# Optimization experiments

Measured on AMD Instinct MI355X. Metric: run time of the kernel, lower is better.

Reference implementation:

```python
import jax, jax.numpy as jnp
import numpy as np

BN_EPS = 1e-5


def setup_inputs() -> dict:
    key = jax.random.key(0)
    ks = jax.random.split(key, 10)
    B, C, H, W = 8, 512, 64, 64      # batch, in_channels, spatial
    K, V, O = 256, 256, 512          # key_channels, value_channels, out_channels
    s = 0.02
    return {
        "x": jax.random.normal(ks[0], (B, C, H, W), jnp.float32),
        # 1x1 convs are channel matmuls: weight [out_c, in_c]
        "wv": jax.random.normal(ks[1], (V, C), jnp.float32) * s,
        "bv": jax.random.normal(ks[2], (V,), jnp.float32) * s,
        "wk": jax.random.normal(ks[3], (K, C), jnp.float32) * s,
        "bk": jax.random.normal(ks[4], (K,), jnp.float32) * s,
        # BatchNorm2d (inference mode: running stats)
        "gamma": jnp.ones((K,), jnp.float32),
        "beta": jnp.zeros((K,), jnp.float32),
        "rmean": jax.random.normal(ks[5], (K,), jnp.float32) * 0.1,
        "rvar": jax.random.uniform(ks[6], (K,), jnp.float32, 0.5, 1.5),
        # output 1x1 conv W (zero-init in torch; use small random for a useful baseline)
        "wW": jax.random.normal(ks[7], (O, V), jnp.float32) * s,
        "bW": jax.random.normal(ks[8], (O,), jnp.float32) * s,
    }


def reference(x, wv, bv, wk, bk, gamma, beta, rmean, rvar, wW, bW):
    B, C, H, W = x.shape
    N = H * W
    xf = x.reshape(B, C, N)                                   # [B, C, N]

    # f_value: 1x1 conv -> [B, V, N]
    value = jnp.einsum('vc,bcn->bvn', wv, xf) + bv[:, None]

    # f_key (= f_query, shared module): conv1x1 + BN(inference) + ReLU -> [B, K, N]
    k = jnp.einsum('kc,bcn->bkn', wk, xf) + bk[:, None]
    scale = gamma / jnp.sqrt(rvar + BN_EPS)
    k = (k - rmean[:, None]) * scale[:, None] + beta[:, None]
    k = jax.nn.relu(k)

    # sim_map = query^T @ key * K^-0.5; query == key since f_query is f_key
    Kc = k.shape[1]
    sim = jnp.einsum('bkn,bkm->bnm', k, k) * (Kc ** -0.5)     # [B, N, N]
    sim = jax.nn.softmax(sim, axis=-1)

    # context = sim @ value^T -> [B, V, N]
    ctx = jnp.einsum('bnm,bvm->bvn', sim, value)

    # output 1x1 conv W
    out = jnp.einsum('ov,bvn->bon', wW, ctx) + bW[:, None]    # [B, O, N]
    return out.reshape(B, -1, H, W)
```

## Files before the change

kernel.cpp:

```cpp
#include <hip/hip_runtime.h>
#include <hip/hip_bf16.h>
#include <stdint.h>


typedef __bf16 bf16;
typedef bf16 bf16x4 __attribute__((ext_vector_type(4)));
typedef bf16 bf16x8 __attribute__((ext_vector_type(8)));
typedef float f32x4 __attribute__((ext_vector_type(4)));
typedef float f32x16 __attribute__((ext_vector_type(16)));

#define Bb 8
#define Cc 512
#define Nn 4096
#define Kc 256
#define Vv 256
#define Oo 512
#define BN_EPS 1e-5f
#define QSCALE 0.300280601f

static __device__ __forceinline__ f32x16 mfma32(bf16x8 a, bf16x8 b, f32x16 c) {
    return __builtin_amdgcn_mfma_f32_32x32x16_bf16(a, b, c, 0, 0, 0);
}
static __device__ __forceinline__ unsigned cvtpk(float lo, float hi) {
    unsigned r;
    asm("v_cvt_pk_bf16_f32 %0, %1, %2" : "=v"(r) : "v"(lo), "v"(hi));
    return r;
}
#define GLD16(gp, lp) __builtin_amdgcn_global_load_lds( \
    (const __attribute__((address_space(1))) unsigned int*)(gp), \
    (__attribute__((address_space(3))) unsigned int*)(lp), 16, 0, 0)

__global__ __launch_bounds__(256) void prep_kernel(
        const float* __restrict__ wk, const float* __restrict__ wv,
        const float* __restrict__ wW, const float* __restrict__ bk,
        const float* __restrict__ gamma, const float* __restrict__ beta,
        const float* __restrict__ rmean, const float* __restrict__ rvar,
        bf16* __restrict__ wkv, bf16* __restrict__ wWb, float* __restrict__ shift2) {
    int idx = blockIdx.x * 256 + threadIdx.x;
    if (idx < 131072) {
        int kc = idx >> 9;
        float sc = gamma[kc] * rsqrtf(rvar[kc] + BN_EPS);
        wkv[idx] = (bf16)(wk[idx] * sc);
    } else if (idx < 262144) {
        wkv[idx] = (bf16)(wv[idx - 131072]);
    } else if (idx < 393216) {
        int j = idx - 262144;
        wWb[j] = (bf16)(wW[j]);
    } else if (idx < 393472) {
        int kc = idx - 393216;
        float sc = gamma[kc] * rsqrtf(rvar[kc] + BN_EPS);
        shift2[kc] = (bk[kc] - rmean[kc]) * sc + beta[kc];
    }
}

__global__ __launch_bounds__(256, 2) void proj_kernel(
        const float* __restrict__ x, const bf16* __restrict__ wkv,
        const float* __restrict__ shift2, const float* __restrict__ bv,
        bf16* __restrict__ kT, bf16* __restrict__ val) {
    int tile = blockIdx.x;
    int b = tile >> 6, n0 = (tile & 63) * 64;
    int t = threadIdx.x, w = t >> 6, l = t & 63, li = l & 31, hi = l >> 5;
    int nsub = w & 1, ochalf = w >> 1;
    int n = n0 + nsub * 32 + li;
    int ncol = nsub * 32 + li;

    __shared__ float xs[32][65];
    bf16x8 bfr[32];
    int r = t >> 3, sseg = t & 7;
#pragma unroll
    for (int p = 0; p < 16; ++p) {
        const float* src = x + ((size_t)(b * Cc + p * 32 + r)) * Nn + n0 + sseg * 8;
        float4 v0 = *(const float4*)src;
        float4 v1 = *(const float4*)(src + 4);
        if (p) __syncthreads();
        xs[r][sseg * 8 + 0] = v0.x; xs[r][sseg * 8 + 1] = v0.y;
        xs[r][sseg * 8 + 2] = v0.z; xs[r][sseg * 8 + 3] = v0.w;
        xs[r][sseg * 8 + 4] = v1.x; xs[r][sseg * 8 + 5] = v1.y;
        xs[r][sseg * 8 + 6] = v1.z; xs[r][sseg * 8 + 7] = v1.w;
        __syncthreads();
        bf16x8 e0, e1;
#pragma unroll
        for (int j = 0; j < 8; ++j) {
            e0[j] = (bf16)xs[hi * 8 + j][ncol];
            e1[j] = (bf16)xs[16 + hi * 8 + j][ncol];
        }
        bfr[2 * p] = e0;
        bfr[2 * p + 1] = e1;
    }

    f32x16 Z;
#pragma unroll
    for (int rr = 0; rr < 16; ++rr) Z[rr] = 0.f;

    auto writeout = [&](const f32x16& acc, int ocbase) {
        if (ocbase < 256) {
#pragma unroll
            for (int rq = 0; rq < 4; ++rq) {
                int kc0 = ocbase + rq * 8 + hi * 4;
                bf16x4 o;
#pragma unroll
                for (int rr = 0; rr < 4; ++rr) {
                    float v = acc[rq * 4 + rr] + shift2[kc0 + rr];
                    o[rr] = (bf16)(fmaxf(v, 0.f) * QSCALE);
                }
                *(bf16x4*)(kT + ((size_t)(b * Nn + n)) * Kc + kc0) = o;
            }
        } else {
#pragma unroll
            for (int rq = 0; rq < 4; ++rq)
#pragma unroll
                for (int rr = 0; rr < 4; ++rr) {
                    int vc = ocbase - 256 + rq * 8 + hi * 4 + rr;
                    val[((size_t)(b * Vv + vc)) * Nn + n] = (bf16)(acc[rq * 4 + rr] + bv[vc]);
                }
        }
    };

    for (int ocp = 0; ocp < 4; ++ocp) {
        int base0 = ochalf * 256 + ocp * 64;
        const bf16* a0 = wkv + (size_t)(base0 + li) * Cc + hi * 8;
        const bf16* a1 = a0 + (size_t)32 * Cc;
        f32x16 acc0 = mfma32(*(const bf16x8*)(a0), bfr[0], Z);
        f32x16 acc1 = mfma32(*(const bf16x8*)(a1), bfr[0], Z);
#pragma unroll
        for (int cs = 1; cs < 32; ++cs) {
            acc0 = mfma32(*(const bf16x8*)(a0 + cs * 16), bfr[cs], acc0);
            acc1 = mfma32(*(const bf16x8*)(a1 + cs * 16), bfr[cs], acc1);
        }
        writeout(acc0, base0);
        writeout(acc1, base0 + 32);
    }
}

__global__ __launch_bounds__(256, 2) void flash_kernel(
        const bf16* __restrict__ kT, const bf16* __restrict__ val,
        bf16* __restrict__ ctxP, float* __restrict__ ml) {
    __shared__ __align__(16) char lds[65536];
    const int t = threadIdx.x;
    const int b = blockIdx.x;
    const int s = blockIdx.z;
    const int w = t >> 6, l = t & 63, li = l & 31, hi = l >> 5;
    const int n = blockIdx.y * 128 + w * 32 + li;
    const int m0 = s * (Nn / 2);
    const int NT = (Nn / 2) / 32;

    const bf16* kTb  = kT  + (size_t)b * Nn * Kc;
    const bf16* valb = val + (size_t)b * Vv * Nn;

    const bf16* qrow = kTb + (size_t)n * Kc;
    bf16x8 qf[16];
#pragma unroll
    for (int cs = 0; cs < 16; ++cs) qf[cs] = *(const bf16x8*)(qrow + cs * 16 + hi * 8);

    int koff[4];
#pragma unroll
    for (int j = 0; j < 4; ++j) {
        int r = j * 8 + (t >> 5);
        koff[j] = r * Kc + ((t & 31) ^ r) * 8;
    }
    char* kdst = lds + w * 1024;
    char* vdst = lds + 16384 + w * 1024;

    const int kq = li * 512 + ((li ^ hi) << 4);
    const int pv = hi * 4096 + li * 16;

    f32x16 Z;
#pragma unroll
    for (int r = 0; r < 16; ++r) Z[r] = 0.f;
    f32x16 ctx[8];
#pragma unroll
    for (int vc = 0; vc < 8; ++vc) ctx[vc] = Z;
    float M = -1.0e30f, L = 0.f;

    auto STAGE = [&](int tile, int bb) {
        const bf16* kg = kTb + (size_t)(m0 + tile * 32) * Kc;
        const bf16* vg = valb + (size_t)t * Nn + (m0 + tile * 32);
#pragma unroll
        for (int j = 0; j < 4; ++j) GLD16(kg + koff[j], kdst + bb * 32768 + j * 4096);
#pragma unroll
        for (int j = 0; j < 4; ++j) GLD16(vg + j * 8, vdst + bb * 32768 + j * 4096);
    };

    STAGE(0, 0);
    for (int it = 0; it < NT; ++it) {
        const int bb = it & 1;
        if (it + 1 < NT) {
            STAGE(it + 1, bb ^ 1);
            asm volatile("s_waitcnt vmcnt(8)" ::: "memory");
        } else {
            asm volatile("s_waitcnt vmcnt(0)" ::: "memory");
        }
        __builtin_amdgcn_s_barrier();
        __builtin_amdgcn_sched_barrier(0);
        const char* kb = lds + bb * 32768;
        const char* vb = kb + 16384;

        __builtin_amdgcn_s_setprio(1);
        f32x16 S = mfma32(*(const bf16x8*)(kb + kq), qf[0], Z);
#pragma unroll
        for (int cs = 1; cs < 16; ++cs) {
            bf16x8 a0 = *(const bf16x8*)(kb + (kq ^ (cs << 5)));
            S = mfma32(a0, qf[cs], S);
        }
        __builtin_amdgcn_s_setprio(0);

        float m0a = fmaxf(fmaxf(S[0], S[1]), fmaxf(S[2], S[3]));
        float m0b = fmaxf(fmaxf(S[4], S[5]), fmaxf(S[6], S[7]));
        float m0c = fmaxf(fmaxf(S[8], S[9]), fmaxf(S[10], S[11]));
        float m0d = fmaxf(fmaxf(S[12], S[13]), fmaxf(S[14], S[15]));
        float tmax = fmaxf(fmaxf(m0a, m0b), fmaxf(m0c, m0d));
        tmax = fmaxf(tmax, __shfl_xor(tmax, 32, 64));
        if (__any(tmax > M + 8.f)) {
            float newM = fmaxf(M, tmax);
            float alpha = exp2f(M - newM);
            M = newM;
            L *= alpha;
#pragma unroll
            for (int vc = 0; vc < 8; ++vc) ctx[vc] = ctx[vc] * alpha;
        }
#pragma unroll
        for (int r = 0; r < 16; ++r) S[r] = exp2f(S[r] - M);
        float t0 = (S[0] + S[1]) + (S[2] + S[3]);
        float t1 = (S[4] + S[5]) + (S[6] + S[7]);
        float t2 = (S[8] + S[9]) + (S[10] + S[11]);
        float t3 = (S[12] + S[13]) + (S[14] + S[15]);
        float tsum = (t0 + t1) + (t2 + t3);
        tsum += __shfl_xor(tsum, 32, 64);
        L += tsum;

        unsigned c0 = cvtpk(S[0], S[1]),  c1 = cvtpk(S[2], S[3]);
        unsigned c2 = cvtpk(S[4], S[5]),  c3 = cvtpk(S[6], S[7]);
        unsigned c4 = cvtpk(S[8], S[9]),  c5 = cvtpk(S[10], S[11]);
        unsigned c6 = cvtpk(S[12], S[13]), c7 = cvtpk(S[14], S[15]);
        auto r0 = __builtin_amdgcn_permlane32_swap(c0, c2, false, false);
        auto r1 = __builtin_amdgcn_permlane32_swap(c1, c3, false, false);
        auto r2 = __builtin_amdgcn_permlane32_swap(c4, c6, false, false);
        auto r3 = __builtin_amdgcn_permlane32_swap(c5, c7, false, false);
        union U8 { unsigned u[4]; bf16x8 v; } B1, B2;
        B1.u[0] = r0[0]; B1.u[1] = r1[0]; B1.u[2] = r0[1]; B1.u[3] = r1[1];
        B2.u[0] = r2[0]; B2.u[1] = r3[0]; B2.u[2] = r2[1]; B2.u[3] = r3[1];

        __builtin_amdgcn_s_setprio(1);
#pragma unroll
        for (int vc = 0; vc < 8; ++vc) {
            bf16x8 va = *(const bf16x8*)(vb + pv + vc * 512);
            ctx[vc] = mfma32(va, B1.v, ctx[vc]);
        }
#pragma unroll
        for (int vc = 0; vc < 8; ++vc) {
            bf16x8 va = *(const bf16x8*)(vb + pv + 8192 + vc * 512);
            ctx[vc] = mfma32(va, B2.v, ctx[vc]);
        }
        __builtin_amdgcn_s_setprio(0);
        if (it + 1 < NT) {
            __builtin_amdgcn_sched_barrier(0);
            __builtin_amdgcn_s_barrier();
        }
    }

    size_t idx = (size_t)(s * Bb + b) * Nn + n;
    bf16* crow = ctxP + idx * Vv;
#pragma unroll
    for (int vc = 0; vc < 8; ++vc) {
#pragma unroll
        for (int rq = 0; rq < 4; ++rq) {
            bf16x4 o;
#pragma unroll
            for (int r = 0; r < 4; ++r) o[r] = (bf16)ctx[vc][rq * 4 + r];
            *(bf16x4*)(crow + vc * 32 + rq * 8 + hi * 4) = o;
        }
    }
    if (hi == 0) {
        float2 v; v.x = M; v.y = L;
        *(float2*)(ml + idx * 2) = v;
    }
}

__global__ __launch_bounds__(256, 2) void out_kernel(
        const bf16* __restrict__ ctxP, const float* __restrict__ ml,
        const bf16* __restrict__ wWb, const float* __restrict__ bW,
        float* __restrict__ out) {
    int tile = blockIdx.x;
    int b = tile >> 6, n0 = (tile & 63) * 64;
    int t = threadIdx.x, w = t >> 6, l = t & 63, li = l & 31, hi = l >> 5;
    int nsub = w & 1, ochalf = w >> 1;
    int n = n0 + nsub * 32 + li;

    size_t iA = (size_t)b * Nn + n;
    size_t iB = (size_t)(Bb + b) * Nn + n;
    const bf16* ca = ctxP + iA * Vv + hi * 8;
    const bf16* cb = ctxP + iB * Vv + hi * 8;
    float MA = ml[iA * 2], LA = ml[iA * 2 + 1];
    float MB = ml[iB * 2], LB = ml[iB * 2 + 1];
    float Mx = fmaxf(MA, MB);
    float wA = exp2f(MA - Mx), wB = exp2f(MB - Mx);
    float inv = 1.f / (LA * wA + LB * wB);
    float sA = wA * inv, sB = wB * inv;

    bf16x8 bfr[16];
#pragma unroll
    for (int cs = 0; cs < 16; ++cs) {
        bf16x8 fa = *(const bf16x8*)(ca + cs * 16);
        bf16x8 fb = *(const bf16x8*)(cb + cs * 16);
        bf16x8 o;
#pragma unroll
        for (int j = 0; j < 8; ++j)
            o[j] = (bf16)(sA * (float)fa[j] + sB * (float)fb[j]);
        bfr[cs] = o;
    }

    f32x16 Z;
#pragma unroll
    for (int r = 0; r < 16; ++r) Z[r] = 0.f;

    for (int ocp = 0; ocp < 4; ++ocp) {
        int base0 = ochalf * 256 + ocp * 64;
        const bf16* a0 = wWb + (size_t)(base0 + li) * Vv + hi * 8;
        const bf16* a1 = a0 + (size_t)32 * Vv;
        f32x16 acc0 = mfma32(*(const bf16x8*)(a0), bfr[0], Z);
        f32x16 acc1 = mfma32(*(const bf16x8*)(a1), bfr[0], Z);
#pragma unroll
        for (int cs = 1; cs < 16; ++cs) {
            acc0 = mfma32(*(const bf16x8*)(a0 + cs * 16), bfr[cs], acc0);
            acc1 = mfma32(*(const bf16x8*)(a1 + cs * 16), bfr[cs], acc1);
        }
#pragma unroll
        for (int rq = 0; rq < 4; ++rq)
#pragma unroll
            for (int r = 0; r < 4; ++r) {
                int oc0 = base0 + rq * 8 + hi * 4 + r;
                out[((size_t)(b * Oo + oc0)) * Nn + n] = acc0[rq * 4 + r] + bW[oc0];
                int oc1 = oc0 + 32;
                out[((size_t)(b * Oo + oc1)) * Nn + n] = acc1[rq * 4 + r] + bW[oc1];
            }
    }
}

extern "C" void kernel_launch(void* const* d_in, const int* in_sizes, int n_in,
                              void* d_out, int out_size, void* d_ws, size_t ws_size,
                              hipStream_t stream) {
    const float* x     = (const float*)d_in[0];
    const float* wv    = (const float*)d_in[1];
    const float* bv    = (const float*)d_in[2];
    const float* wk    = (const float*)d_in[3];
    const float* bk    = (const float*)d_in[4];
    const float* gamma = (const float*)d_in[5];
    const float* beta  = (const float*)d_in[6];
    const float* rmean = (const float*)d_in[7];
    const float* rvar  = (const float*)d_in[8];
    const float* wW    = (const float*)d_in[9];
    const float* bW    = (const float*)d_in[10];
    float* out = (float*)d_out;

    char* ws = (char*)d_ws;
    bf16*  ctxP   = (bf16*)(ws + 0);
    bf16*  kTp    = (bf16*)(ws + 33554432);
    bf16*  valp   = (bf16*)(ws + 50331648);
    bf16*  wkv    = (bf16*)(ws + 67108864);
    bf16*  wWb    = (bf16*)(ws + 67633152);
    float* shift2 = (float*)(ws + 67895296);
    float* ml     = (float*)(ws + 68157440);

    prep_kernel<<<dim3(1537), dim3(256), 0, stream>>>(wk, wv, wW, bk, gamma, beta,
                                                      rmean, rvar, wkv, wWb, shift2);
    proj_kernel<<<dim3(512), dim3(256), 0, stream>>>(x, wkv, shift2, bv, kTp, valp);
    flash_kernel<<<dim3(8, 32, 2), dim3(256), 0, stream>>>(kTp, valp, ctxP, ml);
    out_kernel<<<dim3(512), dim3(256), 0, stream>>>(ctxP, ml, wWb, bW, out);
}
```

Before: 279.3 us.

## Software-pipeline P·V of previous tile with QK^T of current tile

```diff
diff --git a/kernel.cpp b/kernel.cpp
--- a/kernel.cpp
+++ b/kernel.cpp
@@ -135,7 +135,7 @@
 __global__ __launch_bounds__(256, 2) void flash_kernel(
         const bf16* __restrict__ kT, const bf16* __restrict__ val,
         bf16* __restrict__ ctxP, float* __restrict__ ml) {
-    __shared__ __align__(16) char lds[65536];
+    __shared__ __align__(16) char lds[81920];
     const int t = threadIdx.x;
     const int b = blockIdx.x;
     const int s = blockIdx.z;
@@ -159,7 +159,7 @@
         koff[j] = r * Kc + ((t & 31) ^ r) * 8;
     }
     char* kdst = lds + w * 1024;
-    char* vdst = lds + 16384 + w * 1024;
+    char* vdst = lds + 32768 + w * 1024;
 
     const int kq = li * 512 + ((li ^ hi) << 4);
     const int pv = hi * 4096 + li * 16;
@@ -172,37 +172,58 @@
     for (int vc = 0; vc < 8; ++vc) ctx[vc] = Z;
     float M = -1.0e30f, L = 0.f;
 
-    auto STAGE = [&](int tile, int bb) {
+    union U8 { unsigned u[4]; bf16x8 v; };
+    U8 B1p, B2p;
+#pragma unroll
+    for (int j = 0; j < 4; ++j) { B1p.u[j] = 0u; B2p.u[j] = 0u; }
+
+    auto STAGE = [&](int tile, int kbb, int vbb) {
         const bf16* kg = kTb + (size_t)(m0 + tile * 32) * Kc;
         const bf16* vg = valb + (size_t)t * Nn + (m0 + tile * 32);
 #pragma unroll
-        for (int j = 0; j < 4; ++j) GLD16(kg + koff[j], kdst + bb * 32768 + j * 4096);
-#pragma unroll
-        for (int j = 0; j < 4; ++j) GLD16(vg + j * 8, vdst + bb * 32768 + j * 4096);
+        for (int j = 0; j < 4; ++j) GLD16(kg + koff[j], kdst + kbb * 16384 + j * 4096);
+#pragma unroll
+        for (int j = 0; j < 4; ++j) GLD16(vg + j * 8, vdst + vbb * 16384 + j * 4096);
     };
 
-    STAGE(0, 0);
+    int vcur = 0, vnxt = 1, vprv = 2;
+    STAGE(0, 0, 0);
     for (int it = 0; it < NT; ++it) {
-        const int bb = it & 1;
+        const int kbb = it & 1;
         if (it + 1 < NT) {
-            STAGE(it + 1, bb ^ 1);
+            STAGE(it + 1, kbb ^ 1, vnxt);
             asm volatile("s_waitcnt vmcnt(8)" ::: "memory");
         } else {
             asm volatile("s_waitcnt vmcnt(0)" ::: "memory");
         }
         __builtin_amdgcn_s_barrier();
         __builtin_amdgcn_sched_barrier(0);
-        const char* kb = lds + bb * 32768;
-        const char* vb = kb + 16384;
+        const char* kb = lds + kbb * 16384;
+        const char* vprev = lds + 32768 + (it ? vprv : vcur) * 16384;
 
         __builtin_amdgcn_s_setprio(1);
-        f32x16 S = mfma32(*(const bf16x8*)(kb + kq), qf[0], Z);
-#pragma unroll
-        for (int cs = 1; cs < 16; ++cs) {
-            bf16x8 a0 = *(const bf16x8*)(kb + (kq ^ (cs << 5)));
-            S = mfma32(a0, qf[cs], S);
+        f32x16 Sa = mfma32(*(const bf16x8*)(kb + kq), qf[0], Z);
+        f32x16 Sb = mfma32(*(const bf16x8*)(kb + (kq ^ 32)), qf[1], Z);
+#pragma unroll
+        for (int cs = 2; cs < 16; cs += 2) {
+            Sa = mfma32(*(const bf16x8*)(kb + (kq ^ (cs << 5))), qf[cs], Sa);
+            Sb = mfma32(*(const bf16x8*)(kb + (kq ^ ((cs + 1) << 5))), qf[cs + 1], Sb);
+        }
+#pragma unroll
+        for (int vc = 0; vc < 8; ++vc) {
+            bf16x8 va = *(const bf16x8*)(vprev + pv + vc * 512);
+            ctx[vc] = mfma32(va, B1p.v, ctx[vc]);
+        }
+#pragma unroll
+        for (int vc = 0; vc < 8; ++vc) {
+            bf16x8 va = *(const bf16x8*)(vprev + pv + 8192 + vc * 512);
+            ctx[vc] = mfma32(va, B2p.v, ctx[vc]);
         }
         __builtin_amdgcn_s_setprio(0);
+        f32x16 S = Sa + Sb;
+        __builtin_amdgcn_sched_barrier(0);
+        if (it + 1 < NT) __builtin_amdgcn_s_barrier();
+        __builtin_amdgcn_sched_barrier(0);
 
         float m0a = fmaxf(fmaxf(S[0], S[1]), fmaxf(S[2], S[3]));
         float m0b = fmaxf(fmaxf(S[4], S[5]), fmaxf(S[6], S[7]));
@@ -236,26 +257,22 @@
         auto r1 = __builtin_amdgcn_permlane32_swap(c1, c3, false, false);
         auto r2 = __builtin_amdgcn_permlane32_swap(c4, c6, false, false);
         auto r3 = __builtin_amdgcn_permlane32_swap(c5, c7, false, false);
-        union U8 { unsigned u[4]; bf16x8 v; } B1, B2;
-        B1.u[0] = r0[0]; B1.u[1] = r1[0]; B1.u[2] = r0[1]; B1.u[3] = r1[1];
-        B2.u[0] = r2[0]; B2.u[1] = r3[0]; B2.u[2] = r2[1]; B2.u[3] = r3[1];
-
-        __builtin_amdgcn_s_setprio(1);
-#pragma unroll
-        for (int vc = 0; vc < 8; ++vc) {
-            bf16x8 va = *(const bf16x8*)(vb + pv + vc * 512);
-            ctx[vc] = mfma32(va, B1.v, ctx[vc]);
-        }
-#pragma unroll
-        for (int vc = 0; vc < 8; ++vc) {
-            bf16x8 va = *(const bf16x8*)(vb + pv + 8192 + vc * 512);
-            ctx[vc] = mfma32(va, B2.v, ctx[vc]);
-        }
-        __builtin_amdgcn_s_setprio(0);
-        if (it + 1 < NT) {
-            __builtin_amdgcn_sched_barrier(0);
-            __builtin_amdgcn_s_barrier();
-        }
+        B1p.u[0] = r0[0]; B1p.u[1] = r1[0]; B1p.u[2] = r0[1]; B1p.u[3] = r1[1];
+        B2p.u[0] = r2[0]; B2p.u[1] = r3[0]; B2p.u[2] = r2[1]; B2p.u[3] = r3[1];
+
+        int tmp = vprv; vprv = vcur; vcur = vnxt; vnxt = tmp;
+    }
+
+    const char* vlast = lds + 32768 + vprv * 16384;
+#pragma unroll
+    for (int vc = 0; vc < 8; ++vc) {
+        bf16x8 va = *(const bf16x8*)(vlast + pv + vc * 512);
+        ctx[vc] = mfma32(va, B1p.v, ctx[vc]);
+    }
+#pragma unroll
+    for (int vc = 0; vc < 8; ++vc) {
+        bf16x8 va = *(const bf16x8*)(vlast + pv + 8192 + vc * 512);
+        ctx[vc] = mfma32(va, B2p.v, ctx[vc]);
     }
 
     size_t idx = (size_t)(s * Bb + b) * Nn + n;
```

New measurement: 316.1 us. 13.2% more time.

## Stream x tiles into LDS with async direct loads and triple buffering

Applied to the files above, without the earlier changes.

```diff
diff --git a/kernel.cpp b/kernel.cpp
--- a/kernel.cpp
+++ b/kernel.cpp
@@ -64,28 +64,36 @@
     int n = n0 + nsub * 32 + li;
     int ncol = nsub * 32 + li;
 
-    __shared__ float xs[32][65];
+    __shared__ __align__(16) float xs[3][64][64];
+    char* ldsb = (char*)xs;
+    const float* xsrc = x + ((size_t)(b * Cc + w * 16 + (l >> 4))) * Nn + n0 + (l & 15) * 4;
+
+    auto STAGE = [&](int q, int b3) {
+#pragma unroll
+        for (int j = 0; j < 4; ++j)
+            GLD16(xsrc + (size_t)(q * 64 + j * 4) * Nn,
+                  ldsb + b3 * 16384 + w * 4096 + j * 1024);
+    };
+
     bf16x8 bfr[32];
-    int r = t >> 3, sseg = t & 7;
-#pragma unroll
-    for (int p = 0; p < 16; ++p) {
-        const float* src = x + ((size_t)(b * Cc + p * 32 + r)) * Nn + n0 + sseg * 8;
-        float4 v0 = *(const float4*)src;
-        float4 v1 = *(const float4*)(src + 4);
-        if (p) __syncthreads();
-        xs[r][sseg * 8 + 0] = v0.x; xs[r][sseg * 8 + 1] = v0.y;
-        xs[r][sseg * 8 + 2] = v0.z; xs[r][sseg * 8 + 3] = v0.w;
-        xs[r][sseg * 8 + 4] = v1.x; xs[r][sseg * 8 + 5] = v1.y;
-        xs[r][sseg * 8 + 6] = v1.z; xs[r][sseg * 8 + 7] = v1.w;
-        __syncthreads();
-        bf16x8 e0, e1;
-#pragma unroll
-        for (int j = 0; j < 8; ++j) {
-            e0[j] = (bf16)xs[hi * 8 + j][ncol];
-            e1[j] = (bf16)xs[16 + hi * 8 + j][ncol];
-        }
-        bfr[2 * p] = e0;
-        bfr[2 * p + 1] = e1;
+    STAGE(0, 0);
+    for (int q = 0; q < 8; ++q) {
+        if (q < 8 - 1) {
+            STAGE(q + 1, (q + 1) % 3);
+            asm volatile("s_waitcnt vmcnt(4)" ::: "memory");
+        } else {
+            asm volatile("s_waitcnt vmcnt(0)" ::: "memory");
+        }
+        __builtin_amdgcn_s_barrier();
+        __builtin_amdgcn_sched_barrier(0);
+        const float (*xb)[64] = xs[q % 3];
+#pragma unroll
+        for (int cs2 = 0; cs2 < 4; ++cs2) {
+            bf16x8 e;
+#pragma unroll
+            for (int j = 0; j < 8; ++j) e[j] = (bf16)xb[cs2 * 16 + hi * 8 + j][ncol];
+            bfr[q * 4 + cs2] = e;
+        }
     }
 
     f32x16 Z;
```

After: 285.0 us. 1.02x slower.
